# Optimization experiments

Measured on AMD Instinct MI355X. Metric: run time of the kernel, lower is better.

Reference implementation:

```python
import jax, jax.numpy as jnp
import numpy as np

THRESHOLD = 0.05

def binarize101(w, threshold):
    # Ternary quantization to {-1, 0, +1}: zero inside the dead-zone [-thr, thr].
    pos = (w > threshold).astype(w.dtype)
    neg = (w < -threshold).astype(w.dtype)
    return pos - neg

def setup_inputs() -> dict:
    key = jax.random.key(0)
    k1, k2, k3 = jax.random.split(key, 3)
    x = jax.random.normal(k1, (8192, 4096), dtype=jnp.float32)
    weight = jax.random.normal(k2, (4096, 4096), dtype=jnp.float32)
    bias = jax.random.normal(k3, (4096,), dtype=jnp.float32)
    return {"x": x, "weight": weight, "bias": bias}

def reference(x, weight, bias):
    wb = binarize101(weight, THRESHOLD)
    # F.linear: x @ wb.T + bias ; x: [N, in], weight: [out, in] -> [N, out]
    return jnp.einsum('ni,oi->no', x, wb) + bias
```

## Files before the change

kernel.cpp:

```cpp
#include <hip/hip_runtime.h>

typedef float floatx4 __attribute__((ext_vector_type(4)));
typedef __bf16 bf16x8 __attribute__((ext_vector_type(8)));
using u16 = unsigned short;
using u32 = unsigned int;

#define GLOBAL_AS __attribute__((address_space(1)))
#define LDS_AS    __attribute__((address_space(3)))

__global__ void cvt_x_kernel(const float* __restrict__ x, u16* __restrict__ xb, int n8) {
  int stride = gridDim.x * blockDim.x;
  for (int i = blockIdx.x * blockDim.x + threadIdx.x; i < n8; i += stride) {
    const float4* p = (const float4*)(x + (size_t)i * 8);
    float4 a = p[0], b = p[1];
    float v[8] = {a.x, a.y, a.z, a.w, b.x, b.y, b.z, b.w};
    u32 r[8];
#pragma unroll
    for (int j = 0; j < 8; ++j) {
      u32 u = __float_as_uint(v[j]);
      r[j] = (u + 0x7FFFu + ((u >> 16) & 1u)) >> 16;
    }
    uint4 o;
    o.x = r[0] | (r[1] << 16);
    o.y = r[2] | (r[3] << 16);
    o.z = r[4] | (r[5] << 16);
    o.w = r[6] | (r[7] << 16);
    *(uint4*)(xb + (size_t)i * 8) = o;
  }
}

__global__ void quant_w_kernel(const float* __restrict__ w, u16* __restrict__ wb, int n8) {
  int stride = gridDim.x * blockDim.x;
  for (int i = blockIdx.x * blockDim.x + threadIdx.x; i < n8; i += stride) {
    const float4* p = (const float4*)(w + (size_t)i * 8);
    float4 a = p[0], b = p[1];
    float v[8] = {a.x, a.y, a.z, a.w, b.x, b.y, b.z, b.w};
    u32 r[8];
#pragma unroll
    for (int j = 0; j < 8; ++j) {
      r[j] = (v[j] > 0.05f) ? 0x3F80u : ((v[j] < -0.05f) ? 0xBF80u : 0u);
    }
    uint4 o;
    o.x = r[0] | (r[1] << 16);
    o.y = r[2] | (r[3] << 16);
    o.z = r[4] | (r[5] << 16);
    o.w = r[6] | (r[7] << 16);
    *(uint4*)(wb + (size_t)i * 8) = o;
  }
}

__global__ __launch_bounds__(512, 2) void gemm_bin_8ph(
    const u16* __restrict__ A, const u16* __restrict__ B,
    const float* __restrict__ bias, float* __restrict__ C,
    int M, int N, int K) {
  __shared__ u16 lds[65536];

  const int tid = threadIdx.x;
  const int w = tid >> 6, l = tid & 63;
  const int wr = w >> 2, wc = w & 3;
  const int r = l & 15, g = l >> 4;

  const int nbn = N >> 8;
  int wg = blockIdx.x;
  const int nwg = gridDim.x;
  if ((nwg & 7) == 0) wg = (wg & 7) * (nwg >> 3) + (wg >> 3);
  const int bm = wg / nbn, bn = wg % nbn;

  const int NSTEPS = K >> 5;

  const size_t Abase = (size_t)(bm * 256 + (tid >> 2)) * K + (tid & 3) * 8;
  const size_t Bbase = (size_t)(bn * 256 + (tid >> 2)) * K + (tid & 3) * 8;
  const size_t chunkStride = (size_t)128 * K;

  const u16* const ldsA = lds + wr * 4096 + r * 32 + g * 8;
  const u16* const ldsB = lds + 8192 + wc * 2048 + r * 32 + g * 8;

  floatx4 acc[8][4] = {};

  for (int u = 0; u < 4; ++u) {
    const int so = u * 16384;
    const u16* ga = A + Abase + (size_t)u * 32;
    const u16* gb = B + Bbase + (size_t)u * 32;
    __builtin_amdgcn_global_load_lds((const GLOBAL_AS void*)ga,
                                     (LDS_AS void*)(lds + so + tid * 8), 16, 0, 0);
    __builtin_amdgcn_global_load_lds((const GLOBAL_AS void*)(ga + chunkStride),
                                     (LDS_AS void*)(lds + so + 4096 + tid * 8), 16, 0, 0);
    __builtin_amdgcn_global_load_lds((const GLOBAL_AS void*)gb,
                                     (LDS_AS void*)(lds + so + 8192 + tid * 8), 16, 0, 0);
    __builtin_amdgcn_global_load_lds((const GLOBAL_AS void*)(gb + chunkStride),
                                     (LDS_AS void*)(lds + so + 12288 + tid * 8), 16, 0, 0);
  }
  asm volatile("s_waitcnt vmcnt(12)" ::: "memory");
  __builtin_amdgcn_s_barrier();

  for (int s = 0; s < NSTEPS; ++s) {
    const int so = (s & 3) * 16384;
    const bool doSt = (s >= 1) && (s + 3 < NSTEPS);
    const int son = ((s + 3) & 3) * 16384;
    const u16* gaN = A + Abase + (size_t)(s + 3) * 32;
    const u16* gbN = B + Bbase + (size_t)(s + 3) * 32;

    bf16x8 af[8], bf0, bf1, bf2, bf3;
#pragma unroll
    for (int m = 0; m < 8; ++m) af[m] = *(const bf16x8*)(ldsA + so + m * 512);
    bf0 = *(const bf16x8*)(ldsB + so + 0 * 512);
    bf1 = *(const bf16x8*)(ldsB + so + 1 * 512);
    if (doSt) {
      __builtin_amdgcn_global_load_lds((const GLOBAL_AS void*)gaN,
                                       (LDS_AS void*)(lds + son + tid * 8), 16, 0, 0);
      __builtin_amdgcn_global_load_lds((const GLOBAL_AS void*)(gaN + chunkStride),
                                       (LDS_AS void*)(lds + son + 4096 + tid * 8), 16, 0, 0);
    }
    __builtin_amdgcn_s_barrier();
    asm volatile("s_waitcnt lgkmcnt(0)" ::: "memory");
    __builtin_amdgcn_sched_barrier(0);
    __builtin_amdgcn_s_setprio(1);
#pragma unroll
    for (int m = 0; m < 8; ++m) {
      acc[m][0] = __builtin_amdgcn_mfma_f32_16x16x32_bf16(af[m], bf0, acc[m][0], 0, 0, 0);
      acc[m][1] = __builtin_amdgcn_mfma_f32_16x16x32_bf16(af[m], bf1, acc[m][1], 0, 0, 0);
    }
    __builtin_amdgcn_s_setprio(0);
    __builtin_amdgcn_s_barrier();

    bf2 = *(const bf16x8*)(ldsB + so + 2 * 512);
    bf3 = *(const bf16x8*)(ldsB + so + 3 * 512);
    if (doSt) {
      __builtin_amdgcn_global_load_lds((const GLOBAL_AS void*)gbN,
                                       (LDS_AS void*)(lds + son + 8192 + tid * 8), 16, 0, 0);
      __builtin_amdgcn_global_load_lds((const GLOBAL_AS void*)(gbN + chunkStride),
                                       (LDS_AS void*)(lds + son + 12288 + tid * 8), 16, 0, 0);
    }
    __builtin_amdgcn_s_barrier();
    asm volatile("s_waitcnt lgkmcnt(0)" ::: "memory");
    __builtin_amdgcn_sched_barrier(0);
    __builtin_amdgcn_s_setprio(1);
#pragma unroll
    for (int m = 0; m < 8; ++m) {
      acc[m][2] = __builtin_amdgcn_mfma_f32_16x16x32_bf16(af[m], bf2, acc[m][2], 0, 0, 0);
      acc[m][3] = __builtin_amdgcn_mfma_f32_16x16x32_bf16(af[m], bf3, acc[m][3], 0, 0, 0);
    }
    __builtin_amdgcn_s_setprio(0);
    if (s + 1 < NSTEPS) {
      if (s + 3 < NSTEPS)      asm volatile("s_waitcnt vmcnt(8)" ::: "memory");
      else if (s + 2 < NSTEPS) asm volatile("s_waitcnt vmcnt(4)" ::: "memory");
      else                     asm volatile("s_waitcnt vmcnt(0)" ::: "memory");
      __builtin_amdgcn_s_barrier();
    }
  }

  const int colb = bn * 256 + wc * 64;
  float bv[4];
#pragma unroll
  for (int n = 0; n < 4; ++n) bv[n] = bias[colb + n * 16 + r];
  const int rowb0 = bm * 256 + wr * 128;
#pragma unroll
  for (int m = 0; m < 8; ++m) {
    const int rowb = rowb0 + m * 16 + g * 4;
#pragma unroll
    for (int n = 0; n < 4; ++n) {
      const int col = colb + n * 16 + r;
      float* cp = C + (size_t)rowb * N + col;
#pragma unroll
      for (int q = 0; q < 4; ++q) cp[(size_t)q * N] = acc[m][n][q] + bv[n];
    }
  }
}

__global__ void gemm_naive_kernel(const float* __restrict__ x, const float* __restrict__ wgt,
                                  const float* __restrict__ bias, float* __restrict__ out,
                                  int M, int N, int K) {
  long long idx = (long long)blockIdx.x * blockDim.x + threadIdx.x;
  if (idx >= (long long)M * N) return;
  int o = (int)(idx % N);
  int m = (int)(idx / N);
  const float* xr = x + (size_t)m * K;
  const float* wr = wgt + (size_t)o * K;
  float s = 0.f;
  for (int i = 0; i < K; ++i) {
    float wv = wr[i];
    float t = (wv > 0.05f) ? 1.f : ((wv < -0.05f) ? -1.f : 0.f);
    s = fmaf(xr[i], t, s);
  }
  out[idx] = s + bias[o];
}

extern "C" void kernel_launch(void* const* d_in, const int* in_sizes, int n_in,
                              void* d_out, int out_size, void* d_ws, size_t ws_size,
                              hipStream_t stream) {
  const float* x    = (const float*)d_in[0];
  const float* wgt  = (const float*)d_in[1];
  const float* bias = (const float*)d_in[2];
  float* out = (float*)d_out;

  const int N = in_sizes[2];
  const int K = in_sizes[1] / N;
  const int M = in_sizes[0] / K;

  const size_t need = ((size_t)M * K + (size_t)N * K) * sizeof(u16);
  if (ws_size >= need && (M % 256 == 0) && (N % 256 == 0) && (K % 32 == 0) && K >= 128) {
    u16* xb = (u16*)d_ws;
    u16* wb = xb + (size_t)M * K;
    const int nx8 = (M * K) / 8;
    const int nw8 = (N * K) / 8;
    cvt_x_kernel<<<2048, 256, 0, stream>>>(x, xb, nx8);
    quant_w_kernel<<<2048, 256, 0, stream>>>(wgt, wb, nw8);
    const int grid = (M / 256) * (N / 256);
    gemm_bin_8ph<<<grid, 512, 0, stream>>>(xb, wb, bias, out, M, N, K);
  } else {
    const long long total = (long long)M * N;
    gemm_naive_kernel<<<(unsigned)((total + 255) / 256), 256, 0, stream>>>(x, wgt, bias, out, M, N, K);
  }
}
```

Measured before the change: 319.3 us.

## Permute global-to-LDS mapping for contiguous fragment reads and rebalance MFMA phases

The global_load_lds addressing is permuted so each 16-row by 32-k fragment lands in LDS in exactly the order MFMA lanes consume it. Each lane then reads a contiguous 16 bytes at l*8, which is meant to avoid LDS bank conflicts on fragment loads. The two MFMA phases are also regrouped: the first phase computes A rows 0-3 against all four B fragments, and the second phase computes A rows 4-7. This spreads the LDS reads more evenly between the barriers. Global loads now cover 64-byte row segments per lane group instead of whole contiguous rows, which may cost some coalescing efficiency.

```diff
diff --git a/kernel.cpp b/kernel.cpp
--- a/kernel.cpp
+++ b/kernel.cpp
@@ -58,7 +58,7 @@
   const int tid = threadIdx.x;
   const int w = tid >> 6, l = tid & 63;
   const int wr = w >> 2, wc = w & 3;
-  const int r = l & 15, g = l >> 4;
+  const int r = l & 15;
 
   const int nbn = N >> 8;
   int wg = blockIdx.x;
@@ -68,12 +68,14 @@
 
   const int NSTEPS = K >> 5;
 
-  const size_t Abase = (size_t)(bm * 256 + (tid >> 2)) * K + (tid & 3) * 8;
-  const size_t Bbase = (size_t)(bn * 256 + (tid >> 2)) * K + (tid & 3) * 8;
+  const int prow = ((tid >> 6) << 4) + (tid & 15);
+  const int pk = ((tid >> 4) & 3) << 3;
+  const size_t Abase = (size_t)(bm * 256 + prow) * K + pk;
+  const size_t Bbase = (size_t)(bn * 256 + prow) * K + pk;
   const size_t chunkStride = (size_t)128 * K;
 
-  const u16* const ldsA = lds + wr * 4096 + r * 32 + g * 8;
-  const u16* const ldsB = lds + 8192 + wc * 2048 + r * 32 + g * 8;
+  const u16* const ldsA = lds + wr * 4096 + l * 8;
+  const u16* const ldsB = lds + 8192 + wc * 2048 + l * 8;
 
   floatx4 acc[8][4] = {};
 
@@ -100,11 +102,11 @@
     const u16* gaN = A + Abase + (size_t)(s + 3) * 32;
     const u16* gbN = B + Bbase + (size_t)(s + 3) * 32;
 
-    bf16x8 af[8], bf0, bf1, bf2, bf3;
-#pragma unroll
-    for (int m = 0; m < 8; ++m) af[m] = *(const bf16x8*)(ldsA + so + m * 512);
-    bf0 = *(const bf16x8*)(ldsB + so + 0 * 512);
-    bf1 = *(const bf16x8*)(ldsB + so + 1 * 512);
+    bf16x8 af[8], bf[4];
+#pragma unroll
+    for (int m = 0; m < 4; ++m) af[m] = *(const bf16x8*)(ldsA + so + m * 512);
+#pragma unroll
+    for (int n = 0; n < 4; ++n) bf[n] = *(const bf16x8*)(ldsB + so + n * 512);
     if (doSt) {
       __builtin_amdgcn_global_load_lds((const GLOBAL_AS void*)gaN,
                                        (LDS_AS void*)(lds + son + tid * 8), 16, 0, 0);
@@ -116,15 +118,15 @@
     __builtin_amdgcn_sched_barrier(0);
     __builtin_amdgcn_s_setprio(1);
 #pragma unroll
-    for (int m = 0; m < 8; ++m) {
-      acc[m][0] = __builtin_amdgcn_mfma_f32_16x16x32_bf16(af[m], bf0, acc[m][0], 0, 0, 0);
-      acc[m][1] = __builtin_amdgcn_mfma_f32_16x16x32_bf16(af[m], bf1, acc[m][1], 0, 0, 0);
-    }
+    for (int m = 0; m < 4; ++m)
+#pragma unroll
+      for (int n = 0; n < 4; ++n)
+        acc[m][n] = __builtin_amdgcn_mfma_f32_16x16x32_bf16(af[m], bf[n], acc[m][n], 0, 0, 0);
     __builtin_amdgcn_s_setprio(0);
     __builtin_amdgcn_s_barrier();
 
-    bf2 = *(const bf16x8*)(ldsB + so + 2 * 512);
-    bf3 = *(const bf16x8*)(ldsB + so + 3 * 512);
+#pragma unroll
+    for (int m = 4; m < 8; ++m) af[m] = *(const bf16x8*)(ldsA + so + m * 512);
     if (doSt) {
       __builtin_amdgcn_global_load_lds((const GLOBAL_AS void*)gbN,
                                        (LDS_AS void*)(lds + son + 8192 + tid * 8), 16, 0, 0);
@@ -136,10 +138,10 @@
     __builtin_amdgcn_sched_barrier(0);
     __builtin_amdgcn_s_setprio(1);
 #pragma unroll
-    for (int m = 0; m < 8; ++m) {
-      acc[m][2] = __builtin_amdgcn_mfma_f32_16x16x32_bf16(af[m], bf2, acc[m][2], 0, 0, 0);
-      acc[m][3] = __builtin_amdgcn_mfma_f32_16x16x32_bf16(af[m], bf3, acc[m][3], 0, 0, 0);
-    }
+    for (int m = 4; m < 8; ++m)
+#pragma unroll
+      for (int n = 0; n < 4; ++n)
+        acc[m][n] = __builtin_amdgcn_mfma_f32_16x16x32_bf16(af[m], bf[n], acc[m][n], 0, 0, 0);
     __builtin_amdgcn_s_setprio(0);
     if (s + 1 < NSTEPS) {
       if (s + 3 < NSTEPS)      asm volatile("s_waitcnt vmcnt(8)" ::: "memory");
@@ -149,6 +151,7 @@
     }
   }
 
+  const int g = l >> 4;
   const int colb = bn * 256 + wc * 64;
   float bv[4];
 #pragma unroll
```

After: 314.0 us. No clear change (-1.6%).
